# Kernel tuning notes

Hardware: AMD Instinct MI355X
Metric: run time of the kernel (lower is better)

## Reference

```python
import jax, jax.numpy as jnp
import numpy as np

LN_EPS = 1e-5
NEG_INF = -1e30


def setup_inputs() -> dict:
    key = jax.random.key(0)
    ks = jax.random.split(key, 8)
    B, S, D_MODEL, Q_IN = 1, 2048, 1024, 512
    HI, DI = 16, 64            # indexer heads / head_dim
    H, DQK, DV = 8, 64, 64     # MLA heads, qk_head_dim, v_head_dim
    return {
        "x": jax.random.normal(ks[0], (B, S, D_MODEL), jnp.float32),
        "q_input": jax.random.normal(ks[1], (B, S, Q_IN), jnp.float32),
        "q": jax.random.normal(ks[2], (B, S, H, DQK), jnp.float32),
        "k": jax.random.normal(ks[3], (B, S, H, DQK), jnp.float32),
        "v": jax.random.normal(ks[4], (B, S, H, DV), jnp.float32),
        "w_q": jax.random.normal(ks[5], (Q_IN, HI * DI), jnp.float32) * (Q_IN ** -0.5),
        "w_k": jax.random.normal(ks[6], (D_MODEL, DI), jnp.float32) * (D_MODEL ** -0.5),
        "ln_g": jnp.ones((DI,), jnp.float32),
        "ln_b": jnp.zeros((DI,), jnp.float32),
        "w_weights": jax.random.normal(ks[7], (D_MODEL, HI), jnp.float32) * (D_MODEL ** -0.5),
        "top_k": 128,
    }


def _indexer_topk(x, q_input, w_q, w_k, ln_g, ln_b, w_weights, top_k):
    """Lightning indexer: per-head relevance scores -> weighted sum -> causal top-k indices."""
    B, S, _ = x.shape
    HI = w_weights.shape[1]
    DI = w_k.shape[1]
    qi = (q_input @ w_q).reshape(B, S, HI, DI)          # bqhd
    ki = x @ w_k                                         # bkd
    mu = ki.mean(-1, keepdims=True)
    var = ((ki - mu) ** 2).mean(-1, keepdims=True)
    ki = (ki - mu) * jax.lax.rsqrt(var + LN_EPS) * ln_g + ln_b
    # per-head weights; scores*w summed over h == (sum_h w*q) . k  (fused, same math)
    w = (x @ w_weights) * (HI ** -0.5)                   # bqh
    q_eff = jnp.einsum("bqhd,bqh->bqd", qi, w) * (DI ** -0.5)
    scores = jnp.einsum("bqd,bkd->bqk", q_eff, ki)       # [B,S,S]
    pos = jnp.arange(S)
    causal = jnp.where(pos[None, :] <= pos[:, None], 0.0, NEG_INF).astype(scores.dtype)
    scores = scores + causal[None]
    return jax.lax.top_k(scores, top_k)[1]               # [B,S,K]


def reference(x, q_input, q, k, v, w_q, w_k, ln_g, ln_b, w_weights, top_k):
    B, S, H, DQK = q.shape
    DV = v.shape[-1]
    idx = _indexer_topk(x, q_input, w_q, w_k, ln_g, ln_b, w_weights, top_k)  # [B,S,K]

    qh = q.transpose(0, 2, 1, 3)   # [B,H,Sq,D]
    kh = k.transpose(0, 2, 1, 3)   # [B,H,Sk,D]
    vh = v.transpose(0, 2, 1, 3)

    def gather(kv, ix):            # kv [Sk,D], ix [Sq,K] -> [Sq,K,D]
        return kv[ix]

    gather_h = jax.vmap(gather, in_axes=(0, None))       # over heads, shared idx
    gather_bh = jax.vmap(gather_h, in_axes=(0, 0))       # over batch
    k_sel = gather_bh(kh, idx)     # [B,H,Sq,K,D]
    v_sel = gather_bh(vh, idx)     # [B,H,Sq,K,Dv]

    att = jnp.einsum("bhqd,bhqkd->bhqk", qh, k_sel) * (DQK ** -0.5)
    pos = jnp.arange(S)
    valid = idx[:, None, :, :] <= pos[None, None, :, None]   # causal validity of gathered idx
    att = jnp.where(valid, att, NEG_INF)
    p = jax.nn.softmax(att, axis=-1)
    out = jnp.einsum("bhqk,bhqkd->bhqd", p, v_sel)
    return out.transpose(0, 2, 1, 3)   # [B,S,H,Dv]
```

## Files before the change

kernel.cpp:

```cpp
#include <hip/hip_runtime.h>
#include <hip/hip_bf16.h>
#include <hip/hip_fp16.h>
#include <math.h>

#define S 2048
#define DM 1024
#define QIN 512
#define HI 16
#define DI 64
#define NH 8
#define TOPK 128
#define LN_EPS 1e-5f
#define KP 8

typedef float f32x4 __attribute__((ext_vector_type(4)));
typedef short s16x8 __attribute__((ext_vector_type(8)));

__device__ __forceinline__ float wave_sum(float v){
#pragma unroll
  for (int o = 32; o; o >>= 1) v += __shfl_xor(v, o);
  return v;
}
__device__ __forceinline__ float wave_max(float v){
#pragma unroll
  for (int o = 32; o; o >>= 1) v = fmaxf(v, __shfl_xor(v, o));
  return v;
}
__device__ __forceinline__ unsigned short f2bf(float x){
  unsigned u = __float_as_uint(x);
  unsigned r = u + 0x7FFFu + ((u >> 16) & 1u);
  return (unsigned short)(r >> 16);
}
__device__ __forceinline__ float bf2f(unsigned short s){
  return __uint_as_float(((unsigned)s) << 16);
}
__device__ __forceinline__ unsigned short f2h(float x){
  return __half_as_ushort(__float2half_rn(x));
}
union UH2 { unsigned int u; __half2 h; };
__device__ __forceinline__ __half2 as_half2(unsigned int u){ UH2 x; x.u = u; return x.h; }

#define MFMA3(ACC, AH, AL, BH, BL) \
  ACC = __builtin_amdgcn_mfma_f32_16x16x32_bf16(AH, BH, ACC, 0, 0, 0); \
  ACC = __builtin_amdgcn_mfma_f32_16x16x32_bf16(AH, BL, ACC, 0, 0, 0); \
  ACC = __builtin_amdgcn_mfma_f32_16x16x32_bf16(AL, BH, ACC, 0, 0, 0);

#define MFMA6(ACC, AH, AM, AL, BH, BM, BL) \
  ACC = __builtin_amdgcn_mfma_f32_16x16x32_bf16(AH, BH, ACC, 0, 0, 0); \
  ACC = __builtin_amdgcn_mfma_f32_16x16x32_bf16(AH, BM, ACC, 0, 0, 0); \
  ACC = __builtin_amdgcn_mfma_f32_16x16x32_bf16(AM, BH, ACC, 0, 0, 0); \
  ACC = __builtin_amdgcn_mfma_f32_16x16x32_bf16(AH, BL, ACC, 0, 0, 0); \
  ACC = __builtin_amdgcn_mfma_f32_16x16x32_bf16(AL, BH, ACC, 0, 0, 0); \
  ACC = __builtin_amdgcn_mfma_f32_16x16x32_bf16(AM, BM, ACC, 0, 0, 0);

__global__ __launch_bounds__(256) void k_f1(const float* __restrict__ x,
                                            const float* __restrict__ wk,
                                            const float* __restrict__ ww,
                                            float* __restrict__ part,
                                            const float* __restrict__ qin,
                                            unsigned short* __restrict__ Ah,
                                            unsigned short* __restrict__ Al,
                                            const float* __restrict__ k,
                                            unsigned short* __restrict__ kh,
                                            const float* __restrict__ v,
                                            unsigned short* __restrict__ vh,
                                            const float* __restrict__ wq,
                                            unsigned short* __restrict__ Bh,
                                            unsigned short* __restrict__ Bl){
  __shared__ float As[32][68];
  __shared__ float Bs[32][84];
  const int bid = blockIdx.x;
  const int t = threadIdx.x;

  if (bid < 256){
    const int kp = bid & 7;
    const int bm = bid >> 3;
    const int m0 = bm * 64;
    const int tm = (t & 15) * 4;
    const int tn = (t >> 4) * 5;
    float acc[4][5];
#pragma unroll
    for (int i = 0; i < 4; i++)
#pragma unroll
      for (int j = 0; j < 5; j++) acc[i][j] = 0.f;

    for (int kb = 0; kb < (DM / KP) / 32; ++kb){
      const int k0 = kp * (DM / KP) + kb * 32;
#pragma unroll
      for (int i = 0; i < 2; i++){
        int u = t + i * 256;
        int m = u >> 3, c4 = u & 7;
        float4 a = *(const float4*)&x[(size_t)(m0 + m) * DM + k0 + c4 * 4];
        As[c4*4+0][m] = a.x; As[c4*4+1][m] = a.y; As[c4*4+2][m] = a.z; As[c4*4+3][m] = a.w;
      }
#pragma unroll
      for (int i = 0; i < 10; i++){
        int u = t + i * 256;
        int kk = u / 80, nn = u % 80;
        float val = (nn < 64) ? wk[(size_t)(k0 + kk) * 64 + nn]
                              : ww[(size_t)(k0 + kk) * 16 + (nn - 64)];
        Bs[kk][nn] = val;
      }
      __syncthreads();
#pragma unroll
      for (int kk = 0; kk < 32; ++kk){
        float4 a = *(const float4*)&As[kk][tm];
        float av[4] = {a.x, a.y, a.z, a.w};
        float bb[5];
#pragma unroll
        for (int j = 0; j < 5; j++) bb[j] = Bs[kk][tn + j];
#pragma unroll
        for (int i = 0; i < 4; i++)
#pragma unroll
          for (int j = 0; j < 5; j++) acc[i][j] = fmaf(av[i], bb[j], acc[i][j]);
      }
      __syncthreads();
    }
    float* dst = part + (size_t)kp * S * 80;
#pragma unroll
    for (int i = 0; i < 4; i++)
#pragma unroll
      for (int j = 0; j < 5; j++)
        dst[(size_t)(m0 + tm + i) * 80 + tn + j] = acc[i][j];
    return;
  }

  if (bid < 256 + 3072){
    const int SEG0 = S * QIN / 4;
    const int SEG1 = S * NH * 64 / 4;
    int id = (bid - 256) * 256 + t;
    if (id < SEG0){
      float4 f = ((const float4*)qin)[id];
      ushort4 h, lo;
      h.x = f2bf(f.x); lo.x = f2bf(f.x - bf2f(h.x));
      h.y = f2bf(f.y); lo.y = f2bf(f.y - bf2f(h.y));
      h.z = f2bf(f.z); lo.z = f2bf(f.z - bf2f(h.z));
      h.w = f2bf(f.w); lo.w = f2bf(f.w - bf2f(h.w));
      ((ushort4*)Ah)[id] = h;
      ((ushort4*)Al)[id] = lo;
    } else if (id < SEG0 + SEG1){
      int j = id - SEG0;
      float4 f = ((const float4*)k)[j];
      ushort4 o;
      o.x = f2h(f.x); o.y = f2h(f.y); o.z = f2h(f.z); o.w = f2h(f.w);
      ((ushort4*)kh)[j] = o;
    } else {
      int j = id - SEG0 - SEG1;
      float4 f = ((const float4*)v)[j];
      ushort4 o;
      o.x = f2h(f.x); o.y = f2h(f.y); o.z = f2h(f.z); o.w = f2h(f.w);
      ((ushort4*)vh)[j] = o;
    }
    return;
  }

  {
    unsigned short (*lh)[33] = (unsigned short(*)[33])&As[0][0];
    unsigned short (*ll)[33] = (unsigned short(*)[33])&Bs[0][0];
    const int b2 = bid - 3328;
    const int k0 = (b2 & 15) * 32;
    const int n0 = (b2 >> 4) * 32;
    const int c = t & 31, r8 = t >> 5;
#pragma unroll
    for (int i = 0; i < 4; ++i){
      int kk = r8 + i * 8;
      float wv = wq[(size_t)(k0 + kk) * 1024 + n0 + c];
      unsigned short h = f2bf(wv);
      lh[c][kk] = h;
      ll[c][kk] = f2bf(wv - bf2f(h));
    }
    __syncthreads();
    const int kk = t & 31, nl = t >> 5;
#pragma unroll
    for (int i = 0; i < 4; ++i){
      int nn = nl + i * 8;
      Bh[(size_t)(n0 + nn) * QIN + k0 + kk] = lh[nn][kk];
      Bl[(size_t)(n0 + nn) * QIN + k0 + kk] = ll[nn][kk];
    }
  }
}

__global__ __launch_bounds__(256) void k_f2(const float* __restrict__ part,
                                            const float* __restrict__ g,
                                            const float* __restrict__ b,
                                            unsigned short* __restrict__ kih,
                                            unsigned short* __restrict__ kim,
                                            unsigned short* __restrict__ kil,
                                            float* __restrict__ wgt,
                                            const unsigned short* __restrict__ Ah,
                                            const unsigned short* __restrict__ Al,
                                            const unsigned short* __restrict__ Bh,
                                            const unsigned short* __restrict__ Bl,
                                            float* __restrict__ qi){
  const int bid = blockIdx.x;
  if (bid < 512){
    const int s = bid * 4 + (threadIdx.x >> 6);
    const int l = threadIdx.x & 63;
    float kv = 0.f;
#pragma unroll
    for (int p = 0; p < KP; p++) kv += part[(size_t)p * S * 80 + (size_t)s * 80 + l];
    float wv = 0.f;
    if (l < 16){
#pragma unroll
      for (int p = 0; p < KP; p++) wv += part[(size_t)p * S * 80 + (size_t)s * 80 + 64 + l];
    }
    float mu = wave_sum(kv) * (1.f / 64.f);
    float d  = kv - mu;
    float var = wave_sum(d * d) * (1.f / 64.f);
    float o = d * (1.f / sqrtf(var + LN_EPS)) * g[l] + b[l];
    unsigned short h = f2bf(o);
    float r1 = o - bf2f(h);
    unsigned short m = f2bf(r1);
    kih[(size_t)s * 64 + l] = h;
    kim[(size_t)s * 64 + l] = m;
    kil[(size_t)s * 64 + l] = f2bf(r1 - bf2f(m));
    if (l < 16) wgt[(size_t)s * 16 + l] = wv * 0.25f;
    return;
  }
  const int b2 = bid - 512;
  const int kp = b2 & 1;
  const int bidx = b2 >> 1;
  const int bn = bidx & 15;
  const int bm = bidx >> 4;
  const int w = threadIdx.x >> 6, l = threadIdx.x & 63;
  const int r = l & 15, kg = l >> 4;
  const int m0 = bm * 64 + (w >> 1) * 32;
  const int n0 = bn * 64 + (w & 1) * 32;
  const int kbase = kp * 256;
  f32x4 acc00 = {0,0,0,0}, acc01 = {0,0,0,0}, acc10 = {0,0,0,0}, acc11 = {0,0,0,0};
  const size_t aoff = (size_t)(m0 + r) * QIN + kbase + kg * 8;
  const size_t boff = (size_t)(n0 + r) * QIN + kbase + kg * 8;
#pragma unroll 4
  for (int k0 = 0; k0 < 256; k0 += 32){
    s16x8 ah0 = *(const s16x8*)(Ah + aoff + k0);
    s16x8 ah1 = *(const s16x8*)(Ah + aoff + 16 * QIN + k0);
    s16x8 al0 = *(const s16x8*)(Al + aoff + k0);
    s16x8 al1 = *(const s16x8*)(Al + aoff + 16 * QIN + k0);
    s16x8 bh0 = *(const s16x8*)(Bh + boff + k0);
    s16x8 bh1 = *(const s16x8*)(Bh + boff + 16 * QIN + k0);
    s16x8 bl0 = *(const s16x8*)(Bl + boff + k0);
    s16x8 bl1 = *(const s16x8*)(Bl + boff + 16 * QIN + k0);
    MFMA3(acc00, ah0, al0, bh0, bl0)
    MFMA3(acc01, ah0, al0, bh1, bl1)
    MFMA3(acc10, ah1, al1, bh0, bl0)
    MFMA3(acc11, ah1, al1, bh1, bl1)
  }
  float* qip = qi + (size_t)kp * S * 1024;
#pragma unroll
  for (int j = 0; j < 4; ++j){
    qip[(size_t)(m0 +  0 + kg * 4 + j) * 1024 + n0 +  0 + r] = acc00[j];
    qip[(size_t)(m0 +  0 + kg * 4 + j) * 1024 + n0 + 16 + r] = acc01[j];
    qip[(size_t)(m0 + 16 + kg * 4 + j) * 1024 + n0 +  0 + r] = acc10[j];
    qip[(size_t)(m0 + 16 + kg * 4 + j) * 1024 + n0 + 16 + r] = acc11[j];
  }
}

__global__ __launch_bounds__(256) void k_f3(const float* __restrict__ qi,
                                            const float* __restrict__ wgt,
                                            unsigned short* __restrict__ qeh,
                                            unsigned short* __restrict__ qem,
                                            unsigned short* __restrict__ qel){
  const int id = blockIdx.x * 256 + threadIdx.x;
  const int s = id >> 6, d = id & 63;
  const float* qiA = qi;
  const float* qiB = qi + (size_t)S * 1024;
  float acc = 0.f;
#pragma unroll
  for (int h = 0; h < 16; h++){
    float qv = qiA[(size_t)s * 1024 + h * 64 + d] + qiB[(size_t)s * 1024 + h * 64 + d];
    acc = fmaf(wgt[(size_t)s * 16 + h], qv, acc);
  }
  acc *= 0.125f;
  unsigned short hh = f2bf(acc);
  float r1 = acc - bf2f(hh);
  unsigned short mm = f2bf(r1);
  qeh[(size_t)s * 64 + d] = hh;
  qem[(size_t)s * 64 + d] = mm;
  qel[(size_t)s * 64 + d] = f2bf(r1 - bf2f(mm));
}

__global__ __launch_bounds__(256) void k_scores(const unsigned short* __restrict__ qeh,
                                                const unsigned short* __restrict__ qem,
                                                const unsigned short* __restrict__ qel,
                                                const unsigned short* __restrict__ kih,
                                                const unsigned short* __restrict__ kim,
                                                const unsigned short* __restrict__ kil,
                                                float* __restrict__ sc){
  const int bj = blockIdx.x, bi = blockIdx.y;
  if (bj > bi) return;
  const int w = threadIdx.x >> 6, l = threadIdx.x & 63;
  const int r = l & 15, kg = l >> 4;
  const int m0 = bi * 64 + (w >> 1) * 32;
  const int n0 = bj * 64 + (w & 1) * 32;
  f32x4 acc00 = {0,0,0,0}, acc01 = {0,0,0,0}, acc10 = {0,0,0,0}, acc11 = {0,0,0,0};
  const size_t aoff = (size_t)(m0 + r) * 64 + kg * 8;
  const size_t boff = (size_t)(n0 + r) * 64 + kg * 8;
#pragma unroll
  for (int k0 = 0; k0 < 64; k0 += 32){
    s16x8 ah0 = *(const s16x8*)(qeh + aoff + k0);
    s16x8 ah1 = *(const s16x8*)(qeh + aoff + 16 * 64 + k0);
    s16x8 am0 = *(const s16x8*)(qem + aoff + k0);
    s16x8 am1 = *(const s16x8*)(qem + aoff + 16 * 64 + k0);
    s16x8 al0 = *(const s16x8*)(qel + aoff + k0);
    s16x8 al1 = *(const s16x8*)(qel + aoff + 16 * 64 + k0);
    s16x8 bh0 = *(const s16x8*)(kih + boff + k0);
    s16x8 bh1 = *(const s16x8*)(kih + boff + 16 * 64 + k0);
    s16x8 bm0 = *(const s16x8*)(kim + boff + k0);
    s16x8 bm1 = *(const s16x8*)(kim + boff + 16 * 64 + k0);
    s16x8 bl0 = *(const s16x8*)(kil + boff + k0);
    s16x8 bl1 = *(const s16x8*)(kil + boff + 16 * 64 + k0);
    MFMA6(acc00, ah0, am0, al0, bh0, bm0, bl0)
    MFMA6(acc01, ah0, am0, al0, bh1, bm1, bl1)
    MFMA6(acc10, ah1, am1, al1, bh0, bm0, bl0)
    MFMA6(acc11, ah1, am1, al1, bh1, bm1, bl1)
  }
#pragma unroll
  for (int j = 0; j < 4; ++j){
    sc[(size_t)(m0 +  0 + kg * 4 + j) * S + n0 +  0 + r] = acc00[j];
    sc[(size_t)(m0 +  0 + kg * 4 + j) * S + n0 + 16 + r] = acc01[j];
    sc[(size_t)(m0 + 16 + kg * 4 + j) * S + n0 +  0 + r] = acc10[j];
    sc[(size_t)(m0 + 16 + kg * 4 + j) * S + n0 + 16 + r] = acc11[j];
  }
}

__global__ __launch_bounds__(256) void k_topk(const float* __restrict__ sc,
                                              int* __restrict__ idx,
                                              int* __restrict__ cnt){
  const int i = blockIdx.x, t = threadIdx.x;
  const int w = t >> 6, l = t & 63;
  const int n = i + 1;
  int* outr = idx + (size_t)i * TOPK;
  if (n <= TOPK){
    for (int m = t; m < n; m += 256) outr[m] = m;
    if (t == 0) cnt[i] = n;
    return;
  }
  __shared__ unsigned int keys[S];
  __shared__ int lA[S];
  __shared__ int lB[S];
  __shared__ int hist[256];
  __shared__ int wtot[4];
  __shared__ int s_b, s_above, s_out, s_m;
  hist[t] = 0;
  if (t == 0) s_out = 0;
  __syncthreads();
  for (int j = t; j < n; j += 256){
    unsigned int u = __float_as_uint(sc[(size_t)i * S + j]);
    unsigned int kk = (u & 0x80000000u) ? ~u : (u | 0x80000000u);
    keys[j] = kk;
    atomicAdd(&hist[kk >> 24], 1);
  }
  __syncthreads();
  int rem = TOPK;
  {
    const int h = hist[t];
    int vsc = h;
#pragma unroll
    for (int off = 1; off < 64; off <<= 1){
      int u = __shfl_down(vsc, off);
      if (l + off < 64) vsc += u;
    }
    if (l == 0) wtot[w] = vsc;
    __syncthreads();
    int later = 0;
#pragma unroll
    for (int ww = 1; ww < 4; ++ww) if (ww > w) later += wtot[ww];
    const int excl = vsc + later - h;
    if (excl < rem && excl + h >= rem){ s_b = t; s_above = excl; }
    __syncthreads();
  }
  int b = s_b;
  rem -= s_above;
  if (t == 0) s_m = 0;
  __syncthreads();
  for (int j = t; j < n; j += 256){
    int by = keys[j] >> 24;
    if (by > b){ int p = atomicAdd(&s_out, 1); outr[p] = j; }
    else if (by == b){ int p = atomicAdd(&s_m, 1); lA[p] = j; }
  }
  __syncthreads();
  int m = s_m;
  int* Lsrc = lA; int* Ldst = lB;
  bool done = false;
  if (m == rem){
    int base = TOPK - rem;
    for (int u = t; u < m; u += 256) outr[base + u] = Lsrc[u];
    done = true;
  }
  for (int p = 2; p >= 0 && !done; --p){
    const int sh = p * 8;
    __syncthreads();
    hist[t] = 0;
    __syncthreads();
    for (int u = t; u < m; u += 256) atomicAdd(&hist[(keys[Lsrc[u]] >> sh) & 255], 1);
    __syncthreads();
    {
      const int h = hist[t];
      int vsc = h;
#pragma unroll
      for (int off = 1; off < 64; off <<= 1){
        int u = __shfl_down(vsc, off);
        if (l + off < 64) vsc += u;
      }
      if (l == 0) wtot[w] = vsc;
      __syncthreads();
      int later = 0;
#pragma unroll
      for (int ww = 1; ww < 4; ++ww) if (ww > w) later += wtot[ww];
      const int excl = vsc + later - h;
      if (excl < rem && excl + h >= rem){ s_b = t; s_above = excl; }
      __syncthreads();
    }
    b = s_b;
    rem -= s_above;
    if (t == 0) s_m = 0;
    __syncthreads();
    for (int u = t; u < m; u += 256){
      int j = Lsrc[u]; int by = (keys[j] >> sh) & 255;
      if (by > b){ int p2 = atomicAdd(&s_out, 1); outr[p2] = j; }
      else if (by == b){ int p2 = atomicAdd(&s_m, 1); Ldst[p2] = j; }
    }
    __syncthreads();
    m = s_m;
    { int* tmp = Lsrc; Lsrc = Ldst; Ldst = tmp; }
    if (m == rem){
      int base = TOPK - rem;
      for (int u = t; u < m; u += 256) outr[base + u] = Lsrc[u];
      done = true;
    }
  }
  if (!done && t == 0){
    int base = TOPK - rem;
    for (int a = 0; a < rem; ++a){
      int mn = 1 << 30, pos = -1;
      for (int u = 0; u < m; ++u){ int j = Lsrc[u]; if (j < mn){ mn = j; pos = u; } }
      outr[base + a] = mn; Lsrc[pos] = 1 << 30;
    }
  }
  if (t == 0) cnt[i] = TOPK;
}

__global__ __launch_bounds__(256) void k_attn(const float* __restrict__ q,
                                              const unsigned short* __restrict__ kh,
                                              const unsigned short* __restrict__ vh,
                                              const int* __restrict__ idx,
                                              const int* __restrict__ cnt,
                                              float* __restrict__ out){
  const int i = blockIdx.x;
  const int w = threadIdx.x >> 6, l = threadIdx.x & 63;
  const int n = cnt[i];
  const int* irow = idx + (size_t)i * TOPK;

  __shared__ int   sidx[4][TOPK];
  __shared__ float sp[4][2][TOPK];

  sidx[w][l]      = (l < n)      ? irow[l]      : 0;
  sidx[w][l + 64] = (l + 64 < n) ? irow[l + 64] : 0;

  const int h0 = 2 * w, h1 = h0 + 1;
  const int g = l >> 3, gl = l & 7;
  const float* qrow = q + (size_t)i * (NH * 64);
  __half2 qa2[4], qb2[4];
  {
    float4 a0 = *(const float4*)&qrow[h0 * 64 + gl * 8];
    float4 a1 = *(const float4*)&qrow[h0 * 64 + gl * 8 + 4];
    float4 b0 = *(const float4*)&qrow[h1 * 64 + gl * 8];
    float4 b1 = *(const float4*)&qrow[h1 * 64 + gl * 8 + 4];
    qa2[0] = __floats2half2_rn(a0.x * 0.125f, a0.y * 0.125f);
    qa2[1] = __floats2half2_rn(a0.z * 0.125f, a0.w * 0.125f);
    qa2[2] = __floats2half2_rn(a1.x * 0.125f, a1.y * 0.125f);
    qa2[3] = __floats2half2_rn(a1.z * 0.125f, a1.w * 0.125f);
    qb2[0] = __floats2half2_rn(b0.x * 0.125f, b0.y * 0.125f);
    qb2[1] = __floats2half2_rn(b0.z * 0.125f, b0.w * 0.125f);
    qb2[2] = __floats2half2_rn(b1.x * 0.125f, b1.y * 0.125f);
    qb2[3] = __floats2half2_rn(b1.z * 0.125f, b1.w * 0.125f);
  }
  asm volatile("" ::: "memory");

#pragma unroll 4
  for (int pass = 0; pass < TOPK / 8; ++pass){
    const int j = pass * 8 + g;
    const size_t base = (size_t)sidx[w][j] * (NH * 64);
    uint4 u0 = *(const uint4*)(kh + base + h0 * 64 + gl * 8);
    uint4 u1 = *(const uint4*)(kh + base + h1 * 64 + gl * 8);
    __half2 acc0 = __floats2half2_rn(0.f, 0.f);
    __half2 acc1 = __floats2half2_rn(0.f, 0.f);
    acc0 = __hfma2(as_half2(u0.x), qa2[0], acc0);
    acc0 = __hfma2(as_half2(u0.y), qa2[1], acc0);
    acc0 = __hfma2(as_half2(u0.z), qa2[2], acc0);
    acc0 = __hfma2(as_half2(u0.w), qa2[3], acc0);
    acc1 = __hfma2(as_half2(u1.x), qb2[0], acc1);
    acc1 = __hfma2(as_half2(u1.y), qb2[1], acc1);
    acc1 = __hfma2(as_half2(u1.z), qb2[2], acc1);
    acc1 = __hfma2(as_half2(u1.w), qb2[3], acc1);
    float d0 = __low2float(acc0) + __high2float(acc0);
    float d1 = __low2float(acc1) + __high2float(acc1);
#pragma unroll
    for (int o = 1; o < 8; o <<= 1){ d0 += __shfl_xor(d0, o); d1 += __shfl_xor(d1, o); }
    if (gl == 0){ sp[w][0][j] = d0; sp[w][1][j] = d1; }
  }
  asm volatile("" ::: "memory");

  const bool v0 = (l < n), v1 = (l + 64 < n);
  {
    float s0 = v0 ? sp[w][0][l] : -1e30f, s1 = v1 ? sp[w][0][l + 64] : -1e30f;
    float m = wave_max(fmaxf(s0, s1));
    float e0 = v0 ? __expf(s0 - m) : 0.f;
    float e1 = v1 ? __expf(s1 - m) : 0.f;
    float inv = 1.f / wave_sum(e0 + e1);
    sp[w][0][l] = e0 * inv;
    sp[w][0][l + 64] = e1 * inv;
  }
  {
    float s0 = v0 ? sp[w][1][l] : -1e30f, s1 = v1 ? sp[w][1][l + 64] : -1e30f;
    float m = wave_max(fmaxf(s0, s1));
    float e0 = v0 ? __expf(s0 - m) : 0.f;
    float e1 = v1 ? __expf(s1 - m) : 0.f;
    float inv = 1.f / wave_sum(e0 + e1);
    sp[w][1][l] = e0 * inv;
    sp[w][1][l + 64] = e1 * inv;
  }
  asm volatile("" ::: "memory");

  const int kq = l >> 4;
  const int hp = (l >> 3) & 1;
  const int d8 = (l & 7) * 8;
  float o8[8] = {0,0,0,0,0,0,0,0};
#pragma unroll 4
  for (int pass = 0; pass < TOPK / 4; ++pass){
    const int j = pass * 4 + kq;
    const size_t base = (size_t)sidx[w][j] * (NH * 64);
    uint4 uv = *(const uint4*)(vh + base + (h0 + hp) * 64 + d8);
    float p = sp[w][hp][j];
    __half2 va = as_half2(uv.x), vb = as_half2(uv.y), vc = as_half2(uv.z), vd = as_half2(uv.w);
    o8[0] = fmaf(p, __low2float(va),  o8[0]);
    o8[1] = fmaf(p, __high2float(va), o8[1]);
    o8[2] = fmaf(p, __low2float(vb),  o8[2]);
    o8[3] = fmaf(p, __high2float(vb), o8[3]);
    o8[4] = fmaf(p, __low2float(vc),  o8[4]);
    o8[5] = fmaf(p, __high2float(vc), o8[5]);
    o8[6] = fmaf(p, __low2float(vd),  o8[6]);
    o8[7] = fmaf(p, __high2float(vd), o8[7]);
  }
#pragma unroll
  for (int e = 0; e < 8; ++e){
    o8[e] += __shfl_xor(o8[e], 16);
    o8[e] += __shfl_xor(o8[e], 32);
  }
  if (l < 16){
    float* dst = &out[(size_t)i * (NH * 64) + (h0 + hp) * 64 + d8];
    *(float4*)dst       = make_float4(o8[0], o8[1], o8[2], o8[3]);
    *(float4*)(dst + 4) = make_float4(o8[4], o8[5], o8[6], o8[7]);
  }
}

extern "C" void kernel_launch(void* const* d_in, const int* in_sizes, int n_in,
                              void* d_out, int out_size, void* d_ws, size_t ws_size,
                              hipStream_t stream){
  const float* x   = (const float*)d_in[0];
  const float* qin = (const float*)d_in[1];
  const float* q   = (const float*)d_in[2];
  const float* k   = (const float*)d_in[3];
  const float* v   = (const float*)d_in[4];
  const float* wq  = (const float*)d_in[5];
  const float* wk  = (const float*)d_in[6];
  const float* lng = (const float*)d_in[7];
  const float* lnb = (const float*)d_in[8];
  const float* ww  = (const float*)d_in[9];
  float* out = (float*)d_out;

  float* ws = (float*)d_ws;
  float* part = ws;
  float* wgt  = ws + 1310720;
  float* qi   = ws + 1343488;
  float* sc   = ws + 5537792;
  int*   idx  = (int*)(ws + 9732096);
  int*   cnt  = (int*)(ws + 9994240);
  unsigned short* kh  = (unsigned short*)(ws + 9996288);
  unsigned short* vh  = (unsigned short*)(ws + 10520576);
  unsigned short* kih = (unsigned short*)(ws + 11044864);
  unsigned short* kim = (unsigned short*)(ws + 11110400);
  unsigned short* kil = (unsigned short*)(ws + 11175936);
  unsigned short* qeh = (unsigned short*)(ws + 11241472);
  unsigned short* qem = (unsigned short*)(ws + 11307008);
  unsigned short* qel = (unsigned short*)(ws + 11372544);
  unsigned short* Ah  = (unsigned short*)(ws + 11438080);
  unsigned short* Al  = (unsigned short*)(ws + 11962368);
  unsigned short* Bh  = (unsigned short*)(ws + 12486656);
  unsigned short* Bl  = (unsigned short*)(ws + 12748800);

  hipLaunchKernelGGL(k_f1,     dim3(3840),   dim3(256), 0, stream,
                     x, wk, ww, part, qin, Ah, Al, k, kh, v, vh, wq, Bh, Bl);
  hipLaunchKernelGGL(k_f2,     dim3(1536),   dim3(256), 0, stream,
                     part, lng, lnb, kih, kim, kil, wgt, Ah, Al, Bh, Bl, qi);
  hipLaunchKernelGGL(k_f3,     dim3(512),    dim3(256), 0, stream,
                     qi, wgt, qeh, qem, qel);
  hipLaunchKernelGGL(k_scores, dim3(32, 32), dim3(256), 0, stream,
                     qeh, qem, qel, kih, kim, kil, sc);
  hipLaunchKernelGGL(k_topk,   dim3(2048),   dim3(256), 0, stream, sc, idx, cnt);
  hipLaunchKernelGGL(k_attn,   dim3(2048),   dim3(256), 0, stream, q, kh, vh, idx, cnt, out);
}
```

Before: 118.1 us.

## Stage q-projection GEMM tiles in LDS and drop split-K partial buffer

The q_input@w_q GEMM in k_f2 now loads 64x64 tiles of the hi/lo bf16 operands into shared memory and runs the MFMA loop over the full K=512, instead of each wave reading fragments straight from global memory with a two-way split-K. Dropping split-K removes the second qi partial buffer, so k_f3 reads one array instead of summing two, and the workspace offsets shrink. The trade is LDS use, two barriers per K step, and fewer blocks (512 instead of 1024 GEMM blocks) with longer serial K loops.

```diff
diff --git a/kernel.cpp b/kernel.cpp
--- a/kernel.cpp
+++ b/kernel.cpp
@@ -12,6 +12,7 @@
 #define TOPK 128
 #define LN_EPS 1e-5f
 #define KP 8
+#define KVSZ (S * NH * 64)
 
 typedef float f32x4 __attribute__((ext_vector_type(4)));
 typedef short s16x8 __attribute__((ext_vector_type(8)));
@@ -127,7 +128,7 @@
 
   if (bid < 256 + 3072){
     const int SEG0 = S * QIN / 4;
-    const int SEG1 = S * NH * 64 / 4;
+    const int SEG1 = KVSZ / 4;
     int id = (bid - 256) * 256 + t;
     if (id < SEG0){
       float4 f = ((const float4*)qin)[id];
@@ -192,10 +193,15 @@
                                             const unsigned short* __restrict__ Bh,
                                             const unsigned short* __restrict__ Bl,
                                             float* __restrict__ qi){
+  __shared__ short Ash[64][72];
+  __shared__ short Asl[64][72];
+  __shared__ short Bsh[64][72];
+  __shared__ short Bsl[64][72];
   const int bid = blockIdx.x;
+  const int t = threadIdx.x;
   if (bid < 512){
-    const int s = bid * 4 + (threadIdx.x >> 6);
-    const int l = threadIdx.x & 63;
+    const int s = bid * 4 + (t >> 6);
+    const int l = t & 63;
     float kv = 0.f;
 #pragma unroll
     for (int p = 0; p < KP; p++) kv += part[(size_t)p * S * 80 + (size_t)s * 80 + l];
@@ -218,40 +224,56 @@
     return;
   }
   const int b2 = bid - 512;
-  const int kp = b2 & 1;
-  const int bidx = b2 >> 1;
-  const int bn = bidx & 15;
-  const int bm = bidx >> 4;
-  const int w = threadIdx.x >> 6, l = threadIdx.x & 63;
+  const int bn = b2 & 15;
+  const int bm = b2 >> 4;
+  const int w = t >> 6, l = t & 63;
   const int r = l & 15, kg = l >> 4;
   const int m0 = bm * 64 + (w >> 1) * 32;
   const int n0 = bn * 64 + (w & 1) * 32;
-  const int kbase = kp * 256;
+  const int mq = (w >> 1) * 32;
+  const int nq = (w & 1) * 32;
+  const int srow = t >> 3;
+  const int scol = (t & 7) * 8;
+
   f32x4 acc00 = {0,0,0,0}, acc01 = {0,0,0,0}, acc10 = {0,0,0,0}, acc11 = {0,0,0,0};
-  const size_t aoff = (size_t)(m0 + r) * QIN + kbase + kg * 8;
-  const size_t boff = (size_t)(n0 + r) * QIN + kbase + kg * 8;
-#pragma unroll 4
-  for (int k0 = 0; k0 < 256; k0 += 32){
-    s16x8 ah0 = *(const s16x8*)(Ah + aoff + k0);
-    s16x8 ah1 = *(const s16x8*)(Ah + aoff + 16 * QIN + k0);
-    s16x8 al0 = *(const s16x8*)(Al + aoff + k0);
-    s16x8 al1 = *(const s16x8*)(Al + aoff + 16 * QIN + k0);
-    s16x8 bh0 = *(const s16x8*)(Bh + boff + k0);
-    s16x8 bh1 = *(const s16x8*)(Bh + boff + 16 * QIN + k0);
-    s16x8 bl0 = *(const s16x8*)(Bl + boff + k0);
-    s16x8 bl1 = *(const s16x8*)(Bl + boff + 16 * QIN + k0);
-    MFMA3(acc00, ah0, al0, bh0, bl0)
-    MFMA3(acc01, ah0, al0, bh1, bl1)
-    MFMA3(acc10, ah1, al1, bh0, bl0)
-    MFMA3(acc11, ah1, al1, bh1, bl1)
-  }
-  float* qip = qi + (size_t)kp * S * 1024;
+
+  for (int kb = 0; kb < QIN / 64; ++kb){
+    const int k0 = kb * 64;
+#pragma unroll
+    for (int i = 0; i < 2; ++i){
+      int row = srow + i * 32;
+      size_t ga = (size_t)(bm * 64 + row) * QIN + k0 + scol;
+      size_t gb = (size_t)(bn * 64 + row) * QIN + k0 + scol;
+      *(s16x8*)&Ash[row][scol] = *(const s16x8*)(Ah + ga);
+      *(s16x8*)&Asl[row][scol] = *(const s16x8*)(Al + ga);
+      *(s16x8*)&Bsh[row][scol] = *(const s16x8*)(Bh + gb);
+      *(s16x8*)&Bsl[row][scol] = *(const s16x8*)(Bl + gb);
+    }
+    __syncthreads();
+#pragma unroll
+    for (int ks = 0; ks < 2; ++ks){
+      const int ko = ks * 32 + kg * 8;
+      s16x8 ah0 = *(const s16x8*)&Ash[mq + r][ko];
+      s16x8 ah1 = *(const s16x8*)&Ash[mq + 16 + r][ko];
+      s16x8 al0 = *(const s16x8*)&Asl[mq + r][ko];
+      s16x8 al1 = *(const s16x8*)&Asl[mq + 16 + r][ko];
+      s16x8 bh0 = *(const s16x8*)&Bsh[nq + r][ko];
+      s16x8 bh1 = *(const s16x8*)&Bsh[nq + 16 + r][ko];
+      s16x8 bl0 = *(const s16x8*)&Bsl[nq + r][ko];
+      s16x8 bl1 = *(const s16x8*)&Bsl[nq + 16 + r][ko];
+      MFMA3(acc00, ah0, al0, bh0, bl0)
+      MFMA3(acc01, ah0, al0, bh1, bl1)
+      MFMA3(acc10, ah1, al1, bh0, bl0)
+      MFMA3(acc11, ah1, al1, bh1, bl1)
+    }
+    __syncthreads();
+  }
 #pragma unroll
   for (int j = 0; j < 4; ++j){
-    qip[(size_t)(m0 +  0 + kg * 4 + j) * 1024 + n0 +  0 + r] = acc00[j];
-    qip[(size_t)(m0 +  0 + kg * 4 + j) * 1024 + n0 + 16 + r] = acc01[j];
-    qip[(size_t)(m0 + 16 + kg * 4 + j) * 1024 + n0 +  0 + r] = acc10[j];
-    qip[(size_t)(m0 + 16 + kg * 4 + j) * 1024 + n0 + 16 + r] = acc11[j];
+    qi[(size_t)(m0 +  0 + kg * 4 + j) * 1024 + n0 +  0 + r] = acc00[j];
+    qi[(size_t)(m0 +  0 + kg * 4 + j) * 1024 + n0 + 16 + r] = acc01[j];
+    qi[(size_t)(m0 + 16 + kg * 4 + j) * 1024 + n0 +  0 + r] = acc10[j];
+    qi[(size_t)(m0 + 16 + kg * 4 + j) * 1024 + n0 + 16 + r] = acc11[j];
   }
 }
 
@@ -262,14 +284,10 @@
                                             unsigned short* __restrict__ qel){
   const int id = blockIdx.x * 256 + threadIdx.x;
   const int s = id >> 6, d = id & 63;
-  const float* qiA = qi;
-  const float* qiB = qi + (size_t)S * 1024;
   float acc = 0.f;
 #pragma unroll
-  for (int h = 0; h < 16; h++){
-    float qv = qiA[(size_t)s * 1024 + h * 64 + d] + qiB[(size_t)s * 1024 + h * 64 + d];
-    acc = fmaf(wgt[(size_t)s * 16 + h], qv, acc);
-  }
+  for (int h = 0; h < 16; h++)
+    acc = fmaf(wgt[(size_t)s * 16 + h], qi[(size_t)s * 1024 + h * 64 + d], acc);
   acc *= 0.125f;
   unsigned short hh = f2bf(acc);
   float r1 = acc - bf2f(hh);
@@ -573,25 +591,25 @@
   float* part = ws;
   float* wgt  = ws + 1310720;
   float* qi   = ws + 1343488;
-  float* sc   = ws + 5537792;
-  int*   idx  = (int*)(ws + 9732096);
-  int*   cnt  = (int*)(ws + 9994240);
-  unsigned short* kh  = (unsigned short*)(ws + 9996288);
-  unsigned short* vh  = (unsigned short*)(ws + 10520576);
-  unsigned short* kih = (unsigned short*)(ws + 11044864);
-  unsigned short* kim = (unsigned short*)(ws + 11110400);
-  unsigned short* kil = (unsigned short*)(ws + 11175936);
-  unsigned short* qeh = (unsigned short*)(ws + 11241472);
-  unsigned short* qem = (unsigned short*)(ws + 11307008);
-  unsigned short* qel = (unsigned short*)(ws + 11372544);
-  unsigned short* Ah  = (unsigned short*)(ws + 11438080);
-  unsigned short* Al  = (unsigned short*)(ws + 11962368);
-  unsigned short* Bh  = (unsigned short*)(ws + 12486656);
-  unsigned short* Bl  = (unsigned short*)(ws + 12748800);
+  float* sc   = ws + 3440640;
+  int*   idx  = (int*)(ws + 7634944);
+  int*   cnt  = (int*)(ws + 7897088);
+  unsigned short* kh  = (unsigned short*)(ws + 7899136);
+  unsigned short* vh  = (unsigned short*)(ws + 8423424);
+  unsigned short* kih = (unsigned short*)(ws + 8947712);
+  unsigned short* kim = (unsigned short*)(ws + 9013248);
+  unsigned short* kil = (unsigned short*)(ws + 9078784);
+  unsigned short* qeh = (unsigned short*)(ws + 9144320);
+  unsigned short* qem = (unsigned short*)(ws + 9209856);
+  unsigned short* qel = (unsigned short*)(ws + 9275392);
+  unsigned short* Ah  = (unsigned short*)(ws + 9340928);
+  unsigned short* Al  = (unsigned short*)(ws + 9865216);
+  unsigned short* Bh  = (unsigned short*)(ws + 10389504);
+  unsigned short* Bl  = (unsigned short*)(ws + 10651648);
 
   hipLaunchKernelGGL(k_f1,     dim3(3840),   dim3(256), 0, stream,
                      x, wk, ww, part, qin, Ah, Al, k, kh, v, vh, wq, Bh, Bl);
-  hipLaunchKernelGGL(k_f2,     dim3(1536),   dim3(256), 0, stream,
+  hipLaunchKernelGGL(k_f2,     dim3(1024),   dim3(256), 0, stream,
                      part, lng, lnb, kih, kim, kil, wgt, Ah, Al, Bh, Bl, qi);
   hipLaunchKernelGGL(k_f3,     dim3(512),    dim3(256), 0, stream,
                      qi, wgt, qeh, qem, qel);
```

Measured after the change: 97.88 us. 17.1% less time.
